# Performance work log

Hardware: AMD Instinct MI355X
Metric: run time of the kernel (lower is better)

## Reference

```python
import jax, jax.numpy as jnp
import numpy as np
import math

B, F, S, D, NH, L, DFF, M = 8, 48, 64, 512, 8, 4, 2048, 64
PERIOD = 30
NEG = -1e9
EPS = 1e-5

def _slopes(n):
    start = 2.0 ** (-2.0 ** -(math.log2(n) - 3))
    return np.array([start * (start ** i) for i in range(n)], dtype=np.float32)

def _biased_mask():  # (NH, F, F): causal mask + periodic ALiBi bias, alibi[i,j] = -((i-j)//period)
    i = np.arange(F)[:, None]; j = np.arange(F)[None, :]
    alibi = -((i - j) // PERIOD).astype(np.float32)
    return jnp.asarray(np.where(j <= i, _slopes(NH)[:, None, None] * alibi, NEG).astype(np.float32))

def _ppe():  # (F, D): periodic sinusoidal positional encoding (period 30)
    pos = np.arange(PERIOD, dtype=np.float32)[:, None]
    div = np.exp(np.arange(0, D, 2, dtype=np.float32) * (-math.log(10000.0) / D))
    pe = np.zeros((PERIOD, D), np.float32)
    pe[:, 0::2] = np.sin(pos * div)
    pe[:, 1::2] = np.cos(pos * div)
    return jnp.asarray(np.tile(pe, (F // PERIOD + 1, 1))[:F])

BIASED_MASK = _biased_mask()
PE = _ppe()
MEM_MASK = jnp.where(jnp.eye(F, dtype=bool), 0.0, NEG)  # enc_dec diagonal mask (frame i <-> content i)

def _ln(x, g, b):
    mu = x.mean(-1, keepdims=True)
    var = ((x - mu) ** 2).mean(-1, keepdims=True)
    return (x - mu) * jax.lax.rsqrt(var + EPS) * g + b

def _mha(q, k, v, in_w, in_b, out_w, out_b, nh, mask=None):
    Bq, Tq, d = q.shape
    Tk = k.shape[1]
    dh = d // nh
    wq, wk, wv = jnp.split(in_w, 3, axis=0)
    bq, bk, bv = jnp.split(in_b, 3, axis=0)
    qh = (q @ wq.T + bq).reshape(Bq, Tq, nh, dh).transpose(0, 2, 1, 3)
    kh = (k @ wk.T + bk).reshape(Bq, Tk, nh, dh).transpose(0, 2, 1, 3)
    vh = (v @ wv.T + bv).reshape(Bq, Tk, nh, dh).transpose(0, 2, 1, 3)
    s = jnp.einsum('bhqd,bhkd->bhqk', qh, kh) / jnp.sqrt(jnp.float32(dh))
    if mask is not None:
        s = s + mask
    o = jnp.einsum('bhqk,bhkd->bhqd', jax.nn.softmax(s, axis=-1), vh)
    return o.transpose(0, 2, 1, 3).reshape(Bq, Tq, d) @ out_w.T + out_b

def setup_inputs():
    key = jax.random.key(0)
    ks = iter(jax.random.split(key, 40))
    r = lambda *sh: jax.random.normal(next(ks), sh, jnp.float32) * 0.02
    return dict(
        content_code=jax.random.normal(next(ks), (B, F, D), jnp.float32),
        style_code=jax.random.normal(next(ks), (B, D), jnp.float32),
        style_hiddens=jax.random.normal(next(ks), (B, S, D), jnp.float32),
        init_state=jax.random.normal(next(ks), (B, M), jnp.float32),
        ca_in_w=r(3 * D, D), ca_in_b=r(3 * D), ca_out_w=r(D, D), ca_out_b=r(D),
        se_w=r(D, 2 * D), se_b=r(D),
        mm_w=r(D, M), mm_b=r(D),
        mmr_w=r(M, D), mmr_b=r(M),
        sa_in_w=r(L, 3 * D, D), sa_in_b=r(L, 3 * D), sa_out_w=r(L, D, D), sa_out_b=r(L, D),
        xa_in_w=r(L, 3 * D, D), xa_in_b=r(L, 3 * D), xa_out_w=r(L, D, D), xa_out_b=r(L, D),
        ff1_w=r(L, DFF, D), ff1_b=r(L, DFF), ff2_w=r(L, D, DFF), ff2_b=r(L, D),
        ln_g=jnp.ones((L, 3, D), jnp.float32), ln_b=jnp.zeros((L, 3, D), jnp.float32),
    )

def _forward(content_code, style_code, style_hiddens, init_state,
             ca_in_w, ca_in_b, ca_out_w, ca_out_b, se_w, se_b,
             mm_w, mm_b, mmr_w, mmr_b,
             sa_in_w, sa_in_b, sa_out_w, sa_out_b,
             xa_in_w, xa_in_b, xa_out_w, xa_out_b,
             ff1_w, ff1_b, ff2_w, ff2_b, ln_g, ln_b):
    style_emb_g = style_code[:, None, :]
    # 1-head cross-attn of each content frame against style hiddens; the torch code
    # computes this one query (frame) at a time, which is mathematically identical.
    sel = _mha(content_code, style_hiddens, style_hiddens,
               ca_in_w, ca_in_b, ca_out_w, ca_out_b, 1)  # (B, F, D)

    def emb_new(feat, i):  # style_emb_map(cat([feat, style_emb_l_i])) + global style
        return (jnp.concatenate([feat, sel[:, i:i + 1]], -1) @ se_w.T + se_b) + style_emb_g

    def decoder(x, mem):  # post-norm TransformerDecoder, relu FFN, eval (no dropout)
        T = x.shape[1]
        tgt = BIASED_MASK[None, :, :T, :T]
        mmask = MEM_MASK[:T][None, None]  # (1,1,T,F)
        for l in range(L):
            x = _ln(x + _mha(x, x, x, sa_in_w[l], sa_in_b[l], sa_out_w[l], sa_out_b[l], NH, tgt),
                    ln_g[l, 0], ln_b[l, 0])
            x = _ln(x + _mha(x, mem, mem, xa_in_w[l], xa_in_b[l], xa_out_w[l], xa_out_b[l], NH, mmask),
                    ln_g[l, 1], ln_b[l, 1])
            h = jax.nn.relu(x @ ff1_w[l].T + ff1_b[l]) @ ff2_w[l].T + ff2_b[l]
            x = _ln(x + h, ln_g[l, 2], ln_b[l, 2])
        return x

    dec_emb = emb_new((init_state @ mm_w.T + mm_b)[:, None], 0)  # (B,1,D)
    dec_out = None
    for i in range(F):
        dec_input = dec_emb + PE[:dec_emb.shape[1]]
        dec_out = decoder(dec_input, content_code) @ mmr_w.T + mmr_b  # (B, i+1, M)
        new = dec_out[:, -1:] @ mm_w.T + mm_b
        dec_emb = jnp.concatenate([dec_emb, emb_new(new, i)], axis=1)
    return dec_out, sel

def reference(content_code, style_code, style_hiddens, init_state,
              ca_in_w, ca_in_b, ca_out_w, ca_out_b, se_w, se_b,
              mm_w, mm_b, mmr_w, mmr_b,
              sa_in_w, sa_in_b, sa_out_w, sa_out_b,
              xa_in_w, xa_in_b, xa_out_w, xa_out_b,
              ff1_w, ff1_b, ff2_w, ff2_b, ln_g, ln_b):
    return _forward(content_code, style_code, style_hiddens, init_state,
                    ca_in_w, ca_in_b, ca_out_w, ca_out_b, se_w, se_b,
                    mm_w, mm_b, mmr_w, mmr_b,
                    sa_in_w, sa_in_b, sa_out_w, sa_out_b,
                    xa_in_w, xa_in_b, xa_out_w, xa_out_b,
                    ff1_w, ff1_b, ff2_w, ff2_b, ln_g, ln_b)
```

## Files before the change

kernel.cpp:

```cpp
#include <hip/hip_runtime.h>
#include <hip/hip_fp16.h>


typedef _Float16 h2 __attribute__((ext_vector_type(2)));
__device__ inline h2 u2h(unsigned u){ union{unsigned u; h2 h;} c; c.u=u; return c.h; }
#if __has_builtin(__builtin_amdgcn_fdot2)
__device__ inline float FDOT2(h2 a, h2 b, float c){ return __builtin_amdgcn_fdot2(a, b, c, false); }
#else
__device__ inline float FDOT2(h2 a, h2 b, float c){
  return fmaf((float)a.y, (float)b.y, fmaf((float)a.x, (float)b.x, c));
}
#endif

__device__ inline float aload(const float* p){
  return __hip_atomic_load(p, __ATOMIC_RELAXED, __HIP_MEMORY_SCOPE_AGENT);
}
__device__ inline void astore(float* p, float v){
  __hip_atomic_store(p, v, __ATOMIC_RELAXED, __HIP_MEMORY_SCOPE_AGENT);
}

__device__ inline float dot_f16(const ushort* wrow, const ushort* xh, int n){
  const uint4* w4 = (const uint4*)wrow;
  const uint4* x4 = (const uint4*)xh;
  float a0=0.f, a1=0.f, a2=0.f, a3=0.f;
  #pragma unroll 4
  for (int i=0; i<(n>>3); ++i){
    uint4 w = w4[i], x = x4[i];
    a0 = FDOT2(u2h(w.x), u2h(x.x), a0);
    a1 = FDOT2(u2h(w.y), u2h(x.y), a1);
    a2 = FDOT2(u2h(w.z), u2h(x.z), a2);
    a3 = FDOT2(u2h(w.w), u2h(x.w), a3);
  }
  return (a0+a1)+(a2+a3);
}
__device__ inline float dot_f32(const float* wrow, const float* x, int n){
  const float4* w4 = (const float4*)wrow;
  float a0=0.f, a1=0.f, a2=0.f, a3=0.f;
  #pragma unroll 4
  for (int i=0; i<(n>>2); ++i){
    float4 w = w4[i];
    const float* xp = x + i*4;
    a0 = fmaf(w.x, xp[0], a0); a1 = fmaf(w.y, xp[1], a1);
    a2 = fmaf(w.z, xp[2], a2); a3 = fmaf(w.w, xp[3], a3);
  }
  return (a0+a1)+(a2+a3);
}

__global__ void k_transpose(const float* __restrict__ src, float* __restrict__ dst, int R, int C){
  __shared__ float tile[32][33];
  int cb = blockIdx.x*32, rb = blockIdx.y*32;
  int tx = threadIdx.x, ty = threadIdx.y;
  for (int i=ty; i<32; i+=8) tile[i][tx] = src[(size_t)(rb+i)*C + cb+tx];
  __syncthreads();
  for (int i=ty; i<32; i+=8) dst[(size_t)(cb+i)*R + rb+tx] = tile[tx][i];
}

__global__ void k_casthf(const float* __restrict__ s, __half* __restrict__ d, int n){
  int i = blockIdx.x*256 + threadIdx.x;
  if (i < n) d[i] = __float2half(s[i]);
}

__global__ void k_linear(const float* __restrict__ A, int lda,
                         const float* __restrict__ Wt, int ldw,
                         const float* __restrict__ bias,
                         float* __restrict__ C, int ldc,
                         int O, int Din,
                         size_t aStr, size_t wStr, size_t bStr, size_t cStr){
  __shared__ float xs[8*1024];
  __shared__ float red[4096];
  int tid = threadIdx.x;
  int r0 = blockIdx.y*8;
  int z = blockIdx.z;
  const float* Az = A + (size_t)z*aStr;
  const float* Wz = Wt + (size_t)z*wStr;
  const float* Bz = bias ? bias + (size_t)z*bStr : nullptr;
  float* Cz = C + (size_t)z*cStr;
  for (int idx=tid; idx<8*Din; idx+=256){
    int ri = idx / Din, d = idx - ri*Din;
    xs[idx] = Az[(size_t)(r0+ri)*lda + d];
  }
  __syncthreads();
  int op = tid & 63, kp = tid >> 6;
  int o = blockIdx.x*128 + op*2;
  int dq = Din >> 2;
  float a0[8] = {0,0,0,0,0,0,0,0}, a1[8] = {0,0,0,0,0,0,0,0};
  for (int d = kp*dq; d < kp*dq+dq; ++d){
    float2 w = *reinterpret_cast<const float2*>(&Wz[(size_t)d*ldw + o]);
    #pragma unroll
    for (int ri=0; ri<8; ++ri){ float x = xs[ri*Din+d]; a0[ri] += x*w.x; a1[ri] += x*w.y; }
  }
  #pragma unroll
  for (int ri=0; ri<8; ++ri){
    red[((kp*64+op)*8+ri)*2]   = a0[ri];
    red[((kp*64+op)*8+ri)*2+1] = a1[ri];
  }
  __syncthreads();
  for (int idx = tid; idx < 1024; idx += 256){
    int ri = idx >> 7, oc = idx & 127;
    int opp = oc >> 1, c = oc & 1;
    float v = red[((0*64+opp)*8+ri)*2 + c] + red[((1*64+opp)*8+ri)*2 + c]
            + red[((2*64+opp)*8+ri)*2 + c] + red[((3*64+opp)*8+ri)*2 + c];
    int oo = blockIdx.x*128 + oc;
    if (Bz) v += Bz[oo];
    Cz[(size_t)(r0+ri)*ldc + oo] = v;
  }
}

__global__ void k_pe(float* __restrict__ pe){
  int idx = blockIdx.x*256 + threadIdx.x;
  int t = idx >> 9, d = idx & 511;
  int p = t % 30;
  int i2 = d & ~1;
  float div = __expf(-(float)i2 * (9.210340371976184f/512.f));
  float ang = (float)p * div;
  pe[idx] = (d & 1) ? cosf(ang) : sinf(ang);
}

__global__ void k_sel_attn(const float* __restrict__ qh, const float* __restrict__ kh,
                           const float* __restrict__ vh, float* __restrict__ o){
  int bf = blockIdx.x;
  int b  = bf / 48;
  int tid = threadIdx.x;
  __shared__ float qs[512];
  __shared__ float ps[64];
  qs[tid] = qh[(size_t)bf*512 + tid];
  qs[tid+256] = qh[(size_t)bf*512 + tid + 256];
  __syncthreads();
  if (tid < 64){
    const float* kr = kh + (size_t)(b*64+tid)*512;
    float a = 0.f;
    for (int d=0; d<512; ++d) a += qs[d]*kr[d];
    ps[tid] = a * 0.04419417382415922f;
  }
  __syncthreads();
  if (tid == 0){
    float m = -1e30f;
    for (int j=0;j<64;++j) m = fmaxf(m, ps[j]);
    float s = 0.f;
    for (int j=0;j<64;++j){ float e = __expf(ps[j]-m); ps[j]=e; s+=e; }
    float iv = 1.f/s;
    for (int j=0;j<64;++j) ps[j] *= iv;
  }
  __syncthreads();
  float a0=0.f, a1=0.f;
  for (int j=0;j<64;++j){
    const float* vr = vh + (size_t)(b*64+j)*512;
    float pj = ps[j];
    a0 += pj*vr[tid]; a1 += pj*vr[tid+256];
  }
  o[(size_t)bf*512+tid] = a0;
  o[(size_t)bf*512+tid+256] = a1;
}

__global__ void k_cat_tail(const float* __restrict__ sel, float* __restrict__ cat){
  int idx = blockIdx.x*256 + threadIdx.x;
  int b = idx >> 9, d = idx & 511;
  cat[b*1024 + 512 + d] = sel[(size_t)(b*48)*512 + d];
}
__global__ void k_add_style(const float* __restrict__ embt, const float* __restrict__ style,
                            float* __restrict__ emb){
  int idx = blockIdx.x*256 + threadIdx.x;
  emb[idx] = embt[idx] + style[idx];
}

struct DP {
  unsigned* fl;
  float* z;
  float* emb;
  const ushort *Wqkv, *Wo, *Wf1, *Wf2;
  const float *xa_c, *pe;
  const float *sa_in_b, *sa_out_b, *ff1_b, *ff2_b;
  const float *mmr_w, *mmr_b, *mm_w, *mm_b, *se_w, *se_b;
  const float *ln_g, *ln_b, *style, *sel;
  float* dec_out;
};

__launch_bounds__(512, 2)
__global__ void k_decode(DP p){
  const int tid = threadIdx.x;
  const int i = blockIdx.x;
  const int role = ((i & 7) << 1) | ((i >> 3) & 1);
  const int b = i >> 4;
  const int h = role >> 1, half = role & 1;
  const float slope = exp2f(-(float)(h+1));

  __shared__ float kc[4*48*65];
  __shared__ float vs[4*48*64];
  __shared__ float xs[512];
  __shared__ float red[512];
  __shared__ float qs[64], ps[64], d64[64];
  __shared__ float ns[512];
  __shared__ float lnred[16];
  __shared__ __align__(16) __half xhh[512];
  __shared__ __align__(16) __half anh[64];
  __shared__ __align__(16) __half hsh[128];

  unsigned* flb = p.fl + (size_t)b*48*9*16;
  float* zb = p.z + (size_t)b*48*8*512;

  auto waitz = [&](int t, int s, const float* src)->float{
    const unsigned* c = flb + (size_t)(t*9+s)*16;
    while (__hip_atomic_load(c, __ATOMIC_RELAXED, __HIP_MEMORY_SCOPE_AGENT) < 16u)
      __builtin_amdgcn_s_sleep(1);
    return aload(src + tid);
  };
  auto post = [&](int t, int s){
    __syncthreads();
    if (tid == 0)
      __hip_atomic_fetch_add(flb + (size_t)(t*9+s)*16, 1u,
                             __ATOMIC_RELAXED, __HIP_MEMORY_SCOPE_AGENT);
  };
  auto lnorm = [&](float v, const float* g, const float* bb,
                   float* out, __half* oh)->float{
    float s = v, q = v*v;
    #pragma unroll
    for (int off=32; off>0; off>>=1){ s += __shfl_xor(s, off, 64); q += __shfl_xor(q, off, 64); }
    if ((tid & 63) == 0){ lnred[tid>>6] = s; lnred[8+(tid>>6)] = q; }
    __syncthreads();
    s = 0.f; q = 0.f;
    #pragma unroll
    for (int w=0; w<8; ++w){ s += lnred[w]; q += lnred[8+w]; }
    float mu = s * (1.f/512.f);
    float rs = rsqrtf(q*(1.f/512.f) - mu*mu + 1e-5f);
    float r = (v-mu)*rs*g[tid] + bb[tid];
    if (out) out[tid] = r;
    if (oh) oh[tid] = __float2half(r);
    __syncthreads();
    return r;
  };

  for (int t=0; t<48; ++t){
    for (int l=0; l<4; ++l){
      const float* xac = p.xa_c + ((size_t)l*384 + b*48 + t)*512;
      float xa = xac[tid];

      if (l == 0){
        float pe0 = p.pe[t*512+tid];
        float e;
        if (t > 0) e = waitz(t-1, 8, p.emb + ((size_t)t*8+b)*512);
        else       e = aload(p.emb + ((size_t)t*8+b)*512 + tid);
        float x = e + pe0;
        xs[tid] = x; xhh[tid] = __float2half(x);
        __syncthreads();
      } else {
        float z = waitz(t, (l-1)*2+1, zb + ((size_t)t*8 + (l-1)*2+1)*512);
        lnorm(z, p.ln_g + ((l-1)*3+2)*512, p.ln_b + ((l-1)*3+2)*512, xs, xhh);
      }
      if (tid < 384){
        int row = tid >> 1, piece = tid & 1;
        int sec = row >> 6, dch = row & 63;
        int wrow = sec*512 + h*64 + dch;
        float acc = dot_f16(p.Wqkv + ((size_t)l*1536+wrow)*512 + piece*256,
                            (const ushort*)xhh + piece*256, 256);
        acc += __shfl_xor(acc, 1, 64);
        if (piece == 0){
          acc += p.sa_in_b[l*1536+wrow];
          if (sec == 0) qs[dch] = acc;
          else if (sec == 1) kc[(l*48+t)*65 + dch] = acc;
          else vs[(l*48+t)*64 + dch] = acc;
        }
      }
      __syncthreads();
      if (tid < 64){
        float sc = -1e30f;
        if (tid <= t){
          float a = 0.f;
          const float* kr = &kc[(l*48+tid)*65];
          #pragma unroll
          for (int d=0; d<64; ++d) a = fmaf(qs[d], kr[d], a);
          sc = a*0.125f - ((t-tid) >= 30 ? slope : 0.f);
        }
        float m = sc;
        #pragma unroll
        for (int off=32; off>0; off>>=1) m = fmaxf(m, __shfl_xor(m, off, 64));
        float e = (tid <= t) ? __expf(sc-m) : 0.f;
        float s = e;
        #pragma unroll
        for (int off=32; off>0; off>>=1) s += __shfl_xor(s, off, 64);
        ps[tid] = e / s;
      }
      __syncthreads();
      {
        int d = tid & 63, jq = tid >> 6;
        float a = 0.f;
        for (int j=jq*6; j<jq*6+6; ++j)
          if (j <= t) a = fmaf(ps[j], vs[(l*48+j)*64 + d], a);
        red[tid] = a;
      }
      __syncthreads();
      if (tid < 64){
        float a = red[tid]+red[64+tid]+red[128+tid]+red[192+tid]
                + red[256+tid]+red[320+tid]+red[384+tid]+red[448+tid];
        anh[tid] = __float2half(a);
      }
      __syncthreads();
      {
        int oi = tid >> 1, piece = tid & 1;
        int o = half*256 + oi;
        float acc = dot_f16(p.Wo + (((size_t)l*512+o)*512 + h*64) + piece*32,
                            (const ushort*)anh + piece*32, 32);
        acc += __shfl_xor(acc, 1, 64);
        if (piece == 0){
          if (h == 0) acc += xs[o] + p.sa_out_b[l*512+o];
          unsafeAtomicAdd(zb + ((size_t)t*8 + l*2)*512 + o, acc);
        }
      }
      post(t, l*2);

      float r;
      {
        float z = waitz(t, l*2, zb + ((size_t)t*8 + l*2)*512);
        float w = lnorm(z, p.ln_g + (l*3)*512, p.ln_b + (l*3)*512, nullptr, nullptr);
        float u = w + xa;
        r = lnorm(u, p.ln_g + (l*3+1)*512, p.ln_b + (l*3+1)*512, nullptr, xhh);
      }
      {
        int row = tid >> 2, piece = tid & 3;
        float a = dot_f16(p.Wf1 + ((size_t)l*2048 + role*128 + row)*512 + piece*128,
                          (const ushort*)xhh + piece*128, 128);
        a += __shfl_xor(a, 1, 64);
        a += __shfl_xor(a, 2, 64);
        if (piece == 0)
          hsh[row] = __float2half(fmaxf(a + p.ff1_b[l*2048 + role*128 + row], 0.f));
      }
      __syncthreads();
      {
        float a0 = dot_f16(p.Wf2 + ((size_t)l*512+tid)*2048 + role*128, (const ushort*)hsh, 128);
        if (role == 0) a0 += r + p.ff2_b[l*512+tid];
        unsafeAtomicAdd(zb + ((size_t)t*8 + l*2+1)*512 + tid, a0);
      }
      post(t, l*2+1);
    }

    {
      float z = waitz(t, 7, zb + ((size_t)t*8 + 7)*512);
      lnorm(z, p.ln_g + 11*512, p.ln_b + 11*512, xs, nullptr);
    }
    {
      int o8 = tid >> 3, p8 = tid & 7;
      float a = dot_f32(p.mmr_w + (size_t)o8*512 + p8*64, xs + p8*64, 64);
      a += __shfl_xor(a, 1, 64);
      a += __shfl_xor(a, 2, 64);
      a += __shfl_xor(a, 4, 64);
      if (p8 == 0) d64[o8] = a + p.mmr_b[o8];
    }
    __syncthreads();
    if (role == 0 && tid < 64) p.dec_out[((size_t)b*48+t)*64 + tid] = d64[tid];
    ns[tid] = dot_f32(p.mm_w + (size_t)tid*64, d64, 64) + p.mm_b[tid];
    __syncthreads();
    {
      int o5 = tid >> 4, p16 = tid & 15;
      int o = role*32 + o5;
      float acc = (p16 < 8)
        ? dot_f32(p.se_w + (size_t)o*1024 + p16*64, ns + p16*64, 64)
        : dot_f32(p.se_w + (size_t)o*1024 + p16*64,
                  p.sel + ((size_t)b*48+t)*512 + (p16-8)*64, 64);
      acc += __shfl_xor(acc, 1, 64);
      acc += __shfl_xor(acc, 2, 64);
      acc += __shfl_xor(acc, 4, 64);
      acc += __shfl_xor(acc, 8, 64);
      if (p16 == 0){
        acc += p.se_b[o] + p.style[(size_t)b*512+o];
        astore(p.emb + ((size_t)(t+1)*8+b)*512 + o, acc);
      }
    }
    post(t, 8);
  }
}

extern "C" void kernel_launch(void* const* d_in, const int* in_sizes, int n_in,
                              void* d_out, int out_size, void* d_ws, size_t ws_size,
                              hipStream_t stream){
  (void)in_sizes; (void)n_in; (void)out_size; (void)ws_size;
  const float* content = (const float*)d_in[0];
  const float* style   = (const float*)d_in[1];
  const float* shid    = (const float*)d_in[2];
  const float* init_st = (const float*)d_in[3];
  const float* ca_in_w = (const float*)d_in[4];
  const float* ca_in_b = (const float*)d_in[5];
  const float* ca_out_w= (const float*)d_in[6];
  const float* ca_out_b= (const float*)d_in[7];
  const float* se_w    = (const float*)d_in[8];
  const float* se_b    = (const float*)d_in[9];
  const float* mm_w    = (const float*)d_in[10];
  const float* mm_b    = (const float*)d_in[11];
  const float* mmr_w   = (const float*)d_in[12];
  const float* mmr_b   = (const float*)d_in[13];
  const float* sa_in_w = (const float*)d_in[14];
  const float* sa_in_b = (const float*)d_in[15];
  const float* sa_out_w= (const float*)d_in[16];
  const float* sa_out_b= (const float*)d_in[17];
  const float* xa_in_w = (const float*)d_in[18];
  const float* xa_in_b = (const float*)d_in[19];
  const float* xa_out_w= (const float*)d_in[20];
  const float* xa_out_b= (const float*)d_in[21];
  const float* ff1_w   = (const float*)d_in[22];
  const float* ff1_b   = (const float*)d_in[23];
  const float* ff2_w   = (const float*)d_in[24];
  const float* ff2_b   = (const float*)d_in[25];
  const float* ln_g    = (const float*)d_in[26];
  const float* ln_b    = (const float*)d_in[27];

  float* out = (float*)d_out;
  float* dec_out = out;
  float* sel = out + 8*48*64;

  char* base = (char*)d_ws;
  size_t cur = 0;
  auto alloc = [&](size_t bytes)->char*{
    char* pt = base + cur;
    cur += (bytes + 255) & ~(size_t)255;
    return pt;
  };
  unsigned* fl  = (unsigned*)alloc((size_t)8*48*9*16*4);
  float* zacc   = (float*)alloc((size_t)8*48*8*512*4);
  float* emb    = (float*)alloc((size_t)49*8*512*4);
  size_t zero_span = cur;
  ushort* WqkvH = (ushort*)alloc((size_t)4*1536*512*2);
  ushort* WoH   = (ushort*)alloc((size_t)4*512*512*2);
  ushort* Wf1H  = (ushort*)alloc((size_t)4*2048*512*2);
  ushort* Wf2H  = (ushort*)alloc((size_t)4*512*2048*2);
  float* Wt_mm    = (float*)alloc((size_t)64*512*4);
  float* Wt_se    = (float*)alloc((size_t)1024*512*4);
  float* Wt_ca_in = (float*)alloc((size_t)512*1536*4);
  float* Wt_ca_out= (float*)alloc((size_t)512*512*4);
  float* Wt_xa_v  = (float*)alloc((size_t)4*512*512*4);
  float* Wt_xa_o  = (float*)alloc((size_t)4*512*512*4);
  float* xa_c  = (float*)alloc((size_t)4*384*512*4);
  float* pe    = (float*)alloc((size_t)48*512*4);
  float* qh    = (float*)alloc((size_t)384*512*4);
  float* khb   = (float*)alloc((size_t)512*512*4);
  float* vhb   = (float*)alloc((size_t)512*512*4);
  float* attno = (float*)alloc((size_t)384*512*4);
  float* xtmp4 = (float*)alloc((size_t)4*384*512*4);
  float* catb  = (float*)alloc((size_t)8*1024*4);
  float* embt  = (float*)alloc((size_t)8*512*4);
  (void)vhb;

  hipMemsetAsync(fl, 0, zero_span, stream);

  dim3 tb(32,8);
  k_casthf<<<(4*1536*512+255)/256, 256, 0, stream>>>(sa_in_w, (__half*)WqkvH, 4*1536*512);
  k_casthf<<<(4*512*512+255)/256, 256, 0, stream>>>(sa_out_w, (__half*)WoH,  4*512*512);
  k_casthf<<<(4*2048*512+255)/256, 256, 0, stream>>>(ff1_w,  (__half*)Wf1H, 4*2048*512);
  k_casthf<<<(4*512*2048+255)/256, 256, 0, stream>>>(ff2_w,  (__half*)Wf2H, 4*512*2048);
  for (int l=0; l<4; ++l){
    k_transpose<<<dim3(16,16), tb, 0, stream>>>(xa_in_w + (size_t)l*1536*512 + (size_t)1024*512, Wt_xa_v + (size_t)l*512*512, 512, 512);
    k_transpose<<<dim3(16,16), tb, 0, stream>>>(xa_out_w + (size_t)l*512*512, Wt_xa_o + (size_t)l*512*512, 512, 512);
  }
  k_transpose<<<dim3(16,48), tb, 0, stream>>>(ca_in_w,  Wt_ca_in, 1536, 512);
  k_transpose<<<dim3(16,16), tb, 0, stream>>>(ca_out_w, Wt_ca_out, 512, 512);
  k_transpose<<<dim3(32,16), tb, 0, stream>>>(se_w,  Wt_se, 512, 1024);
  k_transpose<<<dim3(2,16),  tb, 0, stream>>>(mm_w,  Wt_mm, 512, 64);

  k_pe<<<96, 256, 0, stream>>>(pe);

  k_linear<<<dim3(4,48), 256, 0, stream>>>(content, 512, Wt_ca_in, 1536, ca_in_b, qh, 512, 512, 512, 0,0,0,0);
  k_linear<<<dim3(4,64,2), 256, 0, stream>>>(shid, 512, Wt_ca_in + 512, 1536, ca_in_b + 512, khb, 512, 512, 512,
                                             0, 512, 512, (size_t)512*512);
  k_sel_attn<<<384, 256, 0, stream>>>(qh, khb, vhb, attno);
  k_linear<<<dim3(4,48), 256, 0, stream>>>(attno, 512, Wt_ca_out, 512, ca_out_b, sel, 512, 512, 512, 0,0,0,0);

  k_linear<<<dim3(4,48,4), 256, 0, stream>>>(content, 512, Wt_xa_v, 512, xa_in_b + 1024, xtmp4, 512, 512, 512,
                                             0, (size_t)512*512, 1536, (size_t)384*512);
  k_linear<<<dim3(4,48,4), 256, 0, stream>>>(xtmp4, 512, Wt_xa_o, 512, xa_out_b, xa_c, 512, 512, 512,
                                             (size_t)384*512, (size_t)512*512, 512, (size_t)384*512);

  k_linear<<<dim3(4,1), 256, 0, stream>>>(init_st, 64, Wt_mm, 512, mm_b, catb, 1024, 512, 64, 0,0,0,0);
  k_cat_tail<<<16, 256, 0, stream>>>(sel, catb);
  k_linear<<<dim3(4,1), 256, 0, stream>>>(catb, 1024, Wt_se, 512, se_b, embt, 512, 512, 1024, 0,0,0,0);
  k_add_style<<<16, 256, 0, stream>>>(embt, style, emb);

  DP p;
  p.fl = fl; p.z = zacc; p.emb = emb;
  p.Wqkv = WqkvH; p.Wo = WoH; p.Wf1 = Wf1H; p.Wf2 = Wf2H;
  p.xa_c = xa_c; p.pe = pe;
  p.sa_in_b = sa_in_b; p.sa_out_b = sa_out_b; p.ff1_b = ff1_b; p.ff2_b = ff2_b;
  p.mmr_w = mmr_w; p.mmr_b = mmr_b; p.mm_w = mm_w; p.mm_b = mm_b;
  p.se_w = se_w; p.se_b = se_b; p.ln_g = ln_g; p.ln_b = ln_b;
  p.style = style; p.sel = sel; p.dec_out = dec_out;

  k_decode<<<dim3(128), dim3(512), 0, stream>>>(p);
}
```

Baseline: 5.122 ms.

## Prefetch layer weights into registers before flag waits and pad shared vectors

Loads the QKV, FFN1, FFN2 and mmr weight slices into registers before the spin-wait on cross-block flags, so global weight latency overlaps the synchronization stall. Shared-memory activation vectors (xs, xh, ns, sel) get padded layouts to reduce bank conflicts when threads read different chunks. The sel vector is staged into shared memory early. Register pressure rises sharply under launch_bounds(512,2), which risks spills or lower occupancy.

Result: slower. 5.259 ms (+2.7%).

```diff
diff --git a/kernel.cpp b/kernel.cpp
--- a/kernel.cpp
+++ b/kernel.cpp
@@ -19,32 +19,64 @@
   __hip_atomic_store(p, v, __ATOMIC_RELAXED, __HIP_MEMORY_SCOPE_AGENT);
 }
 
-__device__ inline float dot_f16(const ushort* wrow, const ushort* xh, int n){
-  const uint4* w4 = (const uint4*)wrow;
-  const uint4* x4 = (const uint4*)xh;
-  float a0=0.f, a1=0.f, a2=0.f, a3=0.f;
-  #pragma unroll 4
-  for (int i=0; i<(n>>3); ++i){
-    uint4 w = w4[i], x = x4[i];
-    a0 = FDOT2(u2h(w.x), u2h(x.x), a0);
-    a1 = FDOT2(u2h(w.y), u2h(x.y), a1);
-    a2 = FDOT2(u2h(w.z), u2h(x.z), a2);
-    a3 = FDOT2(u2h(w.w), u2h(x.w), a3);
-  }
+#define FD4(w,x) do{ a0=FDOT2(u2h((w).x),u2h((x).x),a0); a1=FDOT2(u2h((w).y),u2h((x).y),a1); \
+                     a2=FDOT2(u2h((w).z),u2h((x).z),a2); a3=FDOT2(u2h((w).w),u2h((x).w),a3);}while(0)
+
+__device__ inline float dot128s(const ushort* wrow, const ushort* xh){
+  const uint4* w4=(const uint4*)wrow; const uint4* x4=(const uint4*)xh;
+  float a0=0.f,a1=0.f,a2=0.f,a3=0.f;
+  #pragma unroll
+  for(int i=0;i<16;++i){ uint4 w=w4[i], x=x4[i]; FD4(w,x); }
+  return (a0+a1)+(a2+a3);
+}
+__device__ inline float dot128p(const uint4 (&pw)[16], const ushort* xh){
+  const uint4* x4=(const uint4*)xh;
+  float a0=0.f,a1=0.f,a2=0.f,a3=0.f;
+  #pragma unroll
+  for(int i=0;i<16;++i){ uint4 w=pw[i], x=x4[i]; FD4(w,x); }
+  return (a0+a1)+(a2+a3);
+}
+__device__ inline float dot128p8(const uint4 (&pw)[8], const ushort* wrow, const ushort* xh){
+  const uint4* w4=(const uint4*)wrow; const uint4* x4=(const uint4*)xh;
+  float a0=0.f,a1=0.f,a2=0.f,a3=0.f;
+  #pragma unroll
+  for(int i=0;i<8;++i){ uint4 w=pw[i], x=x4[i]; FD4(w,x); }
+  #pragma unroll
+  for(int i=8;i<16;++i){ uint4 w=w4[i], x=x4[i]; FD4(w,x); }
+  return (a0+a1)+(a2+a3);
+}
+__device__ inline float dot32s(const ushort* wrow, const ushort* xh){
+  const uint4* w4=(const uint4*)wrow; const uint4* x4=(const uint4*)xh;
+  float a0=0.f,a1=0.f,a2=0.f,a3=0.f;
+  #pragma unroll
+  for(int i=0;i<4;++i){ uint4 w=w4[i], x=x4[i]; FD4(w,x); }
   return (a0+a1)+(a2+a3);
 }
 __device__ inline float dot_f32(const float* wrow, const float* x, int n){
   const float4* w4 = (const float4*)wrow;
-  float a0=0.f, a1=0.f, a2=0.f, a3=0.f;
+  float a0=0.f,a1=0.f,a2=0.f,a3=0.f;
   #pragma unroll 4
   for (int i=0; i<(n>>2); ++i){
-    float4 w = w4[i];
-    const float* xp = x + i*4;
+    float4 w = w4[i]; const float* xp = x + i*4;
     a0 = fmaf(w.x, xp[0], a0); a1 = fmaf(w.y, xp[1], a1);
     a2 = fmaf(w.z, xp[2], a2); a3 = fmaf(w.w, xp[3], a3);
   }
   return (a0+a1)+(a2+a3);
 }
+__device__ inline float dot64f_p8(const float4 (&pw)[8], const float* wrow, const float* x){
+  const float4* w4=(const float4*)wrow;
+  float a0=0.f,a1=0.f,a2=0.f,a3=0.f;
+  #pragma unroll
+  for(int i=0;i<8;++i){ float4 w=pw[i]; const float* xp=x+i*4;
+    a0=fmaf(w.x,xp[0],a0); a1=fmaf(w.y,xp[1],a1); a2=fmaf(w.z,xp[2],a2); a3=fmaf(w.w,xp[3],a3);}
+  #pragma unroll
+  for(int i=8;i<16;++i){ float4 w=w4[i]; const float* xp=x+i*4;
+    a0=fmaf(w.x,xp[0],a0); a1=fmaf(w.y,xp[1],a1); a2=fmaf(w.z,xp[2],a2); a3=fmaf(w.w,xp[3],a3);}
+  return (a0+a1)+(a2+a3);
+}
+
+#define XSP(e) (((e)>>6)*68 + ((e)&63))
+#define XHP(e) (((e)>>7)*136 + ((e)&127))
 
 __global__ void k_transpose(const float* __restrict__ src, float* __restrict__ dst, int R, int C){
   __shared__ float tile[32][33];
@@ -186,12 +218,13 @@
 
   __shared__ float kc[4*48*65];
   __shared__ float vs[4*48*64];
-  __shared__ float xs[512];
+  __shared__ float xsp[8*68];
   __shared__ float red[512];
   __shared__ float qs[64], ps[64], d64[64];
-  __shared__ float ns[512];
+  __shared__ float nsp[8*68];
+  __shared__ float selp[8*68];
   __shared__ float lnred[16];
-  __shared__ __align__(16) __half xhh[512];
+  __shared__ __align__(16) __half xhp[4*136];
   __shared__ __align__(16) __half anh[64];
   __shared__ __align__(16) __half hsh[128];
 
@@ -211,7 +244,7 @@
                              __ATOMIC_RELAXED, __HIP_MEMORY_SCOPE_AGENT);
   };
   auto lnorm = [&](float v, const float* g, const float* bb,
-                   float* out, __half* oh)->float{
+                   bool toXs, bool toXh)->float{
     float s = v, q = v*v;
     #pragma unroll
     for (int off=32; off>0; off>>=1){ s += __shfl_xor(s, off, 64); q += __shfl_xor(q, off, 64); }
@@ -223,8 +256,8 @@
     float mu = s * (1.f/512.f);
     float rs = rsqrtf(q*(1.f/512.f) - mu*mu + 1e-5f);
     float r = (v-mu)*rs*g[tid] + bb[tid];
-    if (out) out[tid] = r;
-    if (oh) oh[tid] = __float2half(r);
+    if (toXs) xsp[XSP(tid)] = r;
+    if (toXh) xhp[XHP(tid)] = __float2half(r);
     __syncthreads();
     return r;
   };
@@ -233,6 +266,19 @@
     for (int l=0; l<4; ++l){
       const float* xac = p.xa_c + ((size_t)l*384 + b*48 + t)*512;
       float xa = xac[tid];
+      if (l == 3) selp[XSP(tid)] = p.sel[((size_t)b*48+t)*512 + tid];
+
+      uint4 wq[16];
+      const ushort* wqbase = nullptr;
+      if (tid < 384){
+        int row = tid >> 1, piece = tid & 1;
+        int sec = row >> 6, dch = row & 63;
+        int wrow = sec*512 + h*64 + dch;
+        wqbase = p.Wqkv + ((size_t)l*1536 + wrow)*512 + piece*256;
+        const uint4* w4 = (const uint4*)wqbase;
+        #pragma unroll
+        for (int k=0; k<16; ++k) wq[k] = w4[k];
+      }
 
       if (l == 0){
         float pe0 = p.pe[t*512+tid];
@@ -240,18 +286,19 @@
         if (t > 0) e = waitz(t-1, 8, p.emb + ((size_t)t*8+b)*512);
         else       e = aload(p.emb + ((size_t)t*8+b)*512 + tid);
         float x = e + pe0;
-        xs[tid] = x; xhh[tid] = __float2half(x);
+        xsp[XSP(tid)] = x; xhp[XHP(tid)] = __float2half(x);
         __syncthreads();
       } else {
         float z = waitz(t, (l-1)*2+1, zb + ((size_t)t*8 + (l-1)*2+1)*512);
-        lnorm(z, p.ln_g + ((l-1)*3+2)*512, p.ln_b + ((l-1)*3+2)*512, xs, xhh);
+        lnorm(z, p.ln_g + ((l-1)*3+2)*512, p.ln_b + ((l-1)*3+2)*512, true, true);
       }
       if (tid < 384){
         int row = tid >> 1, piece = tid & 1;
         int sec = row >> 6, dch = row & 63;
         int wrow = sec*512 + h*64 + dch;
-        float acc = dot_f16(p.Wqkv + ((size_t)l*1536+wrow)*512 + piece*256,
-                            (const ushort*)xhh + piece*256, 256);
+        float acc = dot128p(wq, (const ushort*)(xhp + (2*piece)*136))
+                  + dot128s((const ushort*)wqbase + 128,
+                            (const ushort*)(xhp + (2*piece+1)*136));
         acc += __shfl_xor(acc, 1, 64);
         if (piece == 0){
           acc += p.sa_in_b[l*1536+wrow];
@@ -297,27 +344,38 @@
       {
         int oi = tid >> 1, piece = tid & 1;
         int o = half*256 + oi;
-        float acc = dot_f16(p.Wo + (((size_t)l*512+o)*512 + h*64) + piece*32,
-                            (const ushort*)anh + piece*32, 32);
+        float acc = dot32s((const ushort*)(p.Wo + (((size_t)l*512+o)*512 + h*64) + piece*32),
+                           (const ushort*)anh + piece*32);
         acc += __shfl_xor(acc, 1, 64);
         if (piece == 0){
-          if (h == 0) acc += xs[o] + p.sa_out_b[l*512+o];
+          if (h == 0) acc += xsp[XSP(o)] + p.sa_out_b[l*512+o];
           unsafeAtomicAdd(zb + ((size_t)t*8 + l*2)*512 + o, acc);
         }
+      }
+      uint4 wf1[8], wf2[8];
+      {
+        int row = tid >> 2, piece = tid & 3;
+        const uint4* w4 = (const uint4*)(p.Wf1 + ((size_t)l*2048 + role*128 + row)*512 + piece*128);
+        #pragma unroll
+        for (int k=0; k<8; ++k) wf1[k] = w4[k];
+        const uint4* w42 = (const uint4*)(p.Wf2 + ((size_t)l*512 + tid)*2048 + role*128);
+        #pragma unroll
+        for (int k=0; k<8; ++k) wf2[k] = w42[k];
       }
       post(t, l*2);
 
       float r;
       {
         float z = waitz(t, l*2, zb + ((size_t)t*8 + l*2)*512);
-        float w = lnorm(z, p.ln_g + (l*3)*512, p.ln_b + (l*3)*512, nullptr, nullptr);
+        float w = lnorm(z, p.ln_g + (l*3)*512, p.ln_b + (l*3)*512, false, false);
         float u = w + xa;
-        r = lnorm(u, p.ln_g + (l*3+1)*512, p.ln_b + (l*3+1)*512, nullptr, xhh);
+        r = lnorm(u, p.ln_g + (l*3+1)*512, p.ln_b + (l*3+1)*512, false, true);
       }
       {
         int row = tid >> 2, piece = tid & 3;
-        float a = dot_f16(p.Wf1 + ((size_t)l*2048 + role*128 + row)*512 + piece*128,
-                          (const ushort*)xhh + piece*128, 128);
+        float a = dot128p8(wf1,
+                           (const ushort*)(p.Wf1 + ((size_t)l*2048 + role*128 + row)*512 + piece*128),
+                           (const ushort*)(xhp + piece*136));
         a += __shfl_xor(a, 1, 64);
         a += __shfl_xor(a, 2, 64);
         if (piece == 0)
@@ -325,20 +383,29 @@
       }
       __syncthreads();
       {
-        float a0 = dot_f16(p.Wf2 + ((size_t)l*512+tid)*2048 + role*128, (const ushort*)hsh, 128);
+        float a0 = dot128p8(wf2,
+                            (const ushort*)(p.Wf2 + ((size_t)l*512 + tid)*2048 + role*128),
+                            (const ushort*)hsh);
         if (role == 0) a0 += r + p.ff2_b[l*512+tid];
         unsafeAtomicAdd(zb + ((size_t)t*8 + l*2+1)*512 + tid, a0);
       }
       post(t, l*2+1);
     }
 
+    float4 wm[8];
+    {
+      int o8 = tid >> 3, p8 = tid & 7;
+      const float4* w4 = (const float4*)(p.mmr_w + (size_t)o8*512 + p8*64);
+      #pragma unroll
+      for (int k=0; k<8; ++k) wm[k] = w4[k];
+    }
     {
       float z = waitz(t, 7, zb + ((size_t)t*8 + 7)*512);
-      lnorm(z, p.ln_g + 11*512, p.ln_b + 11*512, xs, nullptr);
+      lnorm(z, p.ln_g + 11*512, p.ln_b + 11*512, true, false);
     }
     {
       int o8 = tid >> 3, p8 = tid & 7;
-      float a = dot_f32(p.mmr_w + (size_t)o8*512 + p8*64, xs + p8*64, 64);
+      float a = dot64f_p8(wm, p.mmr_w + (size_t)o8*512 + p8*64, xsp + p8*68);
       a += __shfl_xor(a, 1, 64);
       a += __shfl_xor(a, 2, 64);
       a += __shfl_xor(a, 4, 64);
@@ -346,15 +413,13 @@
     }
     __syncthreads();
     if (role == 0 && tid < 64) p.dec_out[((size_t)b*48+t)*64 + tid] = d64[tid];
-    ns[tid] = dot_f32(p.mm_w + (size_t)tid*64, d64, 64) + p.mm_b[tid];
+    nsp[XSP(tid)] = dot_f32(p.mm_w + (size_t)tid*64, d64, 64) + p.mm_b[tid];
     __syncthreads();
     {
       int o5 = tid >> 4, p16 = tid & 15;
       int o = role*32 + o5;
-      float acc = (p16 < 8)
-        ? dot_f32(p.se_w + (size_t)o*1024 + p16*64, ns + p16*64, 64)
-        : dot_f32(p.se_w + (size_t)o*1024 + p16*64,
-                  p.sel + ((size_t)b*48+t)*512 + (p16-8)*64, 64);
+      const float* xsrc = (p16 < 8) ? (nsp + p16*68) : (selp + (p16-8)*68);
+      float acc = dot_f32(p.se_w + (size_t)o*1024 + p16*64, xsrc, 64);
       acc += __shfl_xor(acc, 1, 64);
       acc += __shfl_xor(acc, 2, 64);
       acc += __shfl_xor(acc, 4, 64);
```
